# Kernel optimization log

Hardware: AMD Instinct MI355X
Metric: run time of the kernel (lower is better)

The kernel has to match this reference:

```python
import jax, jax.numpy as jnp
import numpy as np

B, S, D, H = 2, 2048, 1024, 16
DK = D // H
ROPE_BASE = 10000.0


def setup_inputs() -> dict:
    key = jax.random.key(0)
    ks = jax.random.split(key, 6)
    x = jax.random.normal(ks[0], (B, S, D), dtype=jnp.float32)
    # causal mask, broadcastable to [B,H,S,S]; masked_fill where mask==0
    mask = jnp.tril(jnp.ones((S, S), dtype=bool))[None, None]
    position_ids = jnp.tile(jnp.arange(S, dtype=jnp.int32)[None, :], (B, 1))
    sc = 1.0 / np.sqrt(D)
    Wq = jax.random.normal(ks[1], (D, D), dtype=jnp.float32) * sc
    Wk = jax.random.normal(ks[2], (D, D), dtype=jnp.float32) * sc
    Wv = jax.random.normal(ks[3], (D, D), dtype=jnp.float32) * sc
    Wo = jax.random.normal(ks[4], (D, D), dtype=jnp.float32) * sc
    bo = jnp.zeros((D,), dtype=jnp.float32)
    return {"x": x, "mask": mask, "position_ids": position_ids,
            "Wq": Wq, "Wk": Wk, "Wv": Wv, "Wo": Wo, "bo": bo}


def _rotate_half(t):
    t1, t2 = t[..., : t.shape[-1] // 2], t[..., t.shape[-1] // 2:]
    return jnp.concatenate((-t2, t1), axis=-1)


def reference(x, mask, position_ids, Wq, Wk, Wv, Wo, bo):
    b, s, d = x.shape
    h, dk = H, DK
    scale = 1.0 / np.sqrt(dk)

    def proj(W):  # torch Linear: x @ W.T -> [b,h,s,dk]
        return (x @ W.T).reshape(b, s, h, dk).transpose(0, 2, 1, 3)

    Q, K, V = proj(Wq), proj(Wk), proj(Wv)

    # rotary tables (computed in fp32, matching RotaryEmbedding)
    inv_freq = 1.0 / (ROPE_BASE ** (jnp.arange(0, dk, 2, dtype=jnp.float32) / dk))
    t = jnp.arange(s, dtype=jnp.float32)
    freqs = jnp.outer(t, inv_freq)            # [s, dk/2]
    emb = jnp.concatenate((freqs, freqs), -1) # [s, dk]
    cos = jnp.cos(emb)[position_ids][:, None]  # [b,1,s,dk]
    sin = jnp.sin(emb)[position_ids][:, None]
    Q = Q * cos + _rotate_half(Q) * sin
    K = K * cos + _rotate_half(K) * sin

    scores = jnp.einsum('bhqd,bhkd->bhqk', Q, K) * scale
    scores = jnp.where(mask, scores, jnp.float32(-1e9))
    attn = jax.nn.softmax(scores, axis=-1)  # dropout is identity in eval
    out = jnp.einsum('bhqk,bhkd->bhqd', attn, V)
    out = out.transpose(0, 2, 1, 3).reshape(b, s, d)
    return out @ Wo.T + bo
```

## Files before the change

### kernel.cpp

```cpp
#include <hip/hip_runtime.h>
#include <hip/hip_bf16.h>
#include <cstdint>

#define BB 2
#define SS 2048
#define DD 1024
#define HH 16
#define DK 64
#define MROWS (BB*SS)
#define NQKV  (3*DD)

typedef __bf16 bf16x8 __attribute__((ext_vector_type(8)));
typedef float  f32x4  __attribute__((ext_vector_type(4)));
typedef float  f32x16 __attribute__((ext_vector_type(16)));
typedef unsigned u32x2 __attribute__((ext_vector_type(2)));

static __device__ __forceinline__ unsigned short f2bf(float f) {
    __bf16 h = (__bf16)f;
    return __builtin_bit_cast(unsigned short, h);
}
static __device__ __forceinline__ float bf2f(unsigned short u) {
    return (float)__builtin_bit_cast(__bf16, u);
}

#define GLOAD16(gsrc, ldst) \
    __builtin_amdgcn_global_load_lds((const __attribute__((address_space(1))) void*)(gsrc), \
                                     (__attribute__((address_space(3))) void*)(ldst), 16, 0, 0)

static __device__ __forceinline__ void pl32_swap(unsigned &x, unsigned &y) {
#if __has_builtin(__builtin_amdgcn_permlane32_swap)
    u32x2 r = __builtin_amdgcn_permlane32_swap(x, y, false, false);
    x = r[0]; y = r[1];
#else
    asm volatile("v_permlane32_swap_b32 %0, %1" : "+v"(x), "+v"(y));
#endif
}
static __device__ __forceinline__ float swap_half(float v, bool hi) {
    unsigned x = __builtin_bit_cast(unsigned, v), y = x;
    pl32_swap(x, y);
    return __builtin_bit_cast(float, hi ? x : y);
}
template<int BASE> static __device__ __forceinline__ bf16x8 cvt_chunk(const f32x16 &p) {
    unsigned x0, y0, x1, y1;
    asm("v_cvt_pk_bf16_f32 %0, %1, %2" : "=v"(x0) : "v"(p[BASE+0]), "v"(p[BASE+1]));
    asm("v_cvt_pk_bf16_f32 %0, %1, %2" : "=v"(y0) : "v"(p[BASE+4]), "v"(p[BASE+5]));
    asm("v_cvt_pk_bf16_f32 %0, %1, %2" : "=v"(x1) : "v"(p[BASE+2]), "v"(p[BASE+3]));
    asm("v_cvt_pk_bf16_f32 %0, %1, %2" : "=v"(y1) : "v"(p[BASE+6]), "v"(p[BASE+7]));
    pl32_swap(x0, y0);
    pl32_swap(x1, y1);
    union { unsigned u[4]; bf16x8 v; } r;
    r.u[0] = x0; r.u[1] = x1; r.u[2] = y0; r.u[3] = y1;
    return r.v;
}

__global__ void cast_all(const float* __restrict__ x,  const float* __restrict__ wq,
                         const float* __restrict__ wk, const float* __restrict__ wv,
                         const float* __restrict__ wo,
                         unsigned short* __restrict__ xb, unsigned short* __restrict__ wqkv,
                         unsigned short* __restrict__ wob)
{
    const int NX = MROWS * DD;
    const int NW = DD * DD;
    const int total = (NX + 4 * NW) / 8;
    for (int i = blockIdx.x * blockDim.x + threadIdx.x; i < total; i += gridDim.x * blockDim.x) {
        int base = i * 8;
        const float* src; unsigned short* dst; int off;
        if      (base < NX)          { src = x;  dst = xb;          off = base; }
        else if (base < NX + NW)     { src = wq; dst = wqkv;        off = base - NX; }
        else if (base < NX + 2*NW)   { src = wk; dst = wqkv + NW;   off = base - NX - NW; }
        else if (base < NX + 3*NW)   { src = wv; dst = wqkv + 2*NW; off = base - NX - 2*NW; }
        else                         { src = wo; dst = wob;         off = base - NX - 3*NW; }
        float4 a = *(const float4*)(src + off);
        float4 b = *(const float4*)(src + off + 4);
        union { unsigned short s[8]; uint4 v; } u;
        u.s[0] = f2bf(a.x); u.s[1] = f2bf(a.y); u.s[2] = f2bf(a.z); u.s[3] = f2bf(a.w);
        u.s[4] = f2bf(b.x); u.s[5] = f2bf(b.y); u.s[6] = f2bf(b.z); u.s[7] = f2bf(b.w);
        *(uint4*)(dst + off) = u.v;
    }
}

__global__ void rope_table(float* __restrict__ tabc, float* __restrict__ tabs)
{
    int i = blockIdx.x * blockDim.x + threadIdx.x;
    int s = i >> 5, d = i & 31;
    float inv = exp2f(-(float)d * (13.287712379549449f / 32.f));
    float ang = (float)s * inv;
    tabc[i] = cosf(ang);
    tabs[i] = sinf(ang);
}

__global__ __launch_bounds__(512) void gemm_qkv(
    const unsigned short* __restrict__ A, const unsigned short* __restrict__ Bm,
    const int* __restrict__ pids,
    const float* __restrict__ tabc, const float* __restrict__ tabs,
    unsigned short* __restrict__ Qb, unsigned short* __restrict__ Kb,
    unsigned short* __restrict__ Vr)
{
    __shared__ __align__(16) unsigned short sA[2][16384];
    __shared__ __align__(16) unsigned short sB[2][16384];
    const int tid = threadIdx.x;
    const int w = tid >> 6, l = tid & 63;
    const int wm = w >> 2, wn = w & 3;
    const int lr = l & 15, lg = l >> 4;
    const int swz = (blockIdx.x & 7) * 24 + (blockIdx.x >> 3);
    const int bx = swz % 12, by = swz / 12;
    const int mBase = by * 256;
    const int sr  = tid >> 3;
    const int scb = (tid & 7) * 8;
    const int sksw = scb ^ ((sr & 7) * 8);
    const int rdsw = (lr & 7) * 8;

    f32x4 acc[8][4] = {};

    auto stage = [&](int kt, int bb) {
        #pragma unroll
        for (int r = 0; r < 4; ++r) {
            GLOAD16(A  + (size_t)(mBase + r*64 + sr) * DD + kt + sksw,
                    &sA[bb][r*4096 + sr*64 + scb]);
            GLOAD16(Bm + (size_t)(bx*256 + r*64 + sr) * DD + kt + sksw,
                    &sB[bb][r*4096 + sr*64 + scb]);
        }
    };

    stage(0, 0);
    __syncthreads();

    for (int t = 0; t < 16; ++t) {
        const int cur = t & 1;
        #pragma unroll
        for (int p = 0; p < 4; ++p) {
            const int rh = p & 1, ks = p >> 1;
            bf16x8 af[4], bfv[4];
            #pragma unroll
            for (int rf = 0; rf < 4; ++rf) {
                int ra = wm*128 + rh*64 + rf*16 + lr;
                af[rf] = *(const bf16x8*)&sA[cur][ra*64 + ((ks*32 + lg*8) ^ rdsw)];
            }
            #pragma unroll
            for (int cf = 0; cf < 4; ++cf) {
                int rb = wn*64 + cf*16 + lr;
                bfv[cf] = *(const bf16x8*)&sB[cur][rb*64 + ((ks*32 + lg*8) ^ rdsw)];
            }
            if (p == 0 && t < 15) stage((t+1)*64, cur ^ 1);
            __builtin_amdgcn_s_barrier();
            __builtin_amdgcn_s_setprio(1);
            #pragma unroll
            for (int rf = 0; rf < 4; ++rf)
                #pragma unroll
                for (int cf = 0; cf < 4; ++cf)
                    acc[rh*4+rf][cf] = __builtin_amdgcn_mfma_f32_16x16x32_bf16(
                        af[rf], bfv[cf], acc[rh*4+rf][cf], 0, 0, 0);
            __builtin_amdgcn_s_setprio(0);
            if (p < 3) __builtin_amdgcn_s_barrier();
        }
        __syncthreads();
    }

    if (bx < 8) {
        const bool isQ = bx < 4;
        unsigned short* dst = isQ ? Qb : Kb;
        const float qsc = isQ ? 0.1803368801111244f : 1.0f;
        const int colbase = (bx & 3)*256 + wn*64;
        #pragma unroll
        for (int rr = 0; rr < 8; ++rr) {
            #pragma unroll
            for (int j = 0; j < 4; ++j) {
                int row = mBase + wm*128 + rr*16 + lg*4 + j;
                int pos = pids[row];
                #pragma unroll
                for (int cf = 0; cf < 2; ++cf) {
                    int d = cf*16 + lr;
                    float cc = tabc[pos*32 + d];
                    float sn = tabs[pos*32 + d];
                    float a  = acc[rr][cf][j];
                    float bb2 = acc[rr][cf+2][j];
                    dst[(size_t)row * DD + colbase + d]      = f2bf((a*cc - bb2*sn) * qsc);
                    dst[(size_t)row * DD + colbase + d + 32] = f2bf((bb2*cc + a*sn) * qsc);
                }
            }
        }
    } else {
        const int colbase = (bx - 8)*256 + wn*64;
        #pragma unroll
        for (int rr = 0; rr < 8; ++rr) {
            #pragma unroll
            for (int j = 0; j < 4; ++j) {
                int row = mBase + wm*128 + rr*16 + lg*4 + j;
                #pragma unroll
                for (int cf = 0; cf < 4; ++cf)
                    Vr[(size_t)row * DD + colbase + cf*16 + lr] = f2bf(acc[rr][cf][j]);
            }
        }
    }
}

__global__ __launch_bounds__(256) void gemm_bt(
    const unsigned short* __restrict__ A, const unsigned short* __restrict__ Bm,
    float* __restrict__ Cout, const float* __restrict__ bias,
    int M, int N, int K)
{
    __shared__ __align__(16) unsigned short sA[2][128 * 64];
    __shared__ __align__(16) unsigned short sB[2][128 * 64];
    const int tid = threadIdx.x;
    const int w = tid >> 6, l = tid & 63;
    const int wm = w >> 1, wn = w & 1;
    const int lr = l & 15, lg = l >> 4;
    const int nwg = gridDim.x;
    const int cpx = nwg >> 3;
    const int swz = (blockIdx.x & 7) * cpx + (blockIdx.x >> 3);
    const int nbx = N >> 7;
    const int bx = swz % nbx, by = swz / nbx;
    const int mBase = by * 128, nBase = bx * 128;
    const int srow = tid >> 3;
    const int skof = (tid & 7) * 8;

    f32x4 acc[4][4] = {};

    #pragma unroll
    for (int i = 0; i < 4; ++i) {
        GLOAD16(A  + (size_t)(mBase + i*32 + srow) * K + skof, &sA[0][i*2048 + w*512]);
        GLOAD16(Bm + (size_t)(nBase + i*32 + srow) * K + skof, &sB[0][i*2048 + w*512]);
    }
    int cur = 0;

    for (int kt = 0; kt < K; kt += 64) {
        __syncthreads();
        if (kt + 64 < K) {
            #pragma unroll
            for (int i = 0; i < 4; ++i) {
                GLOAD16(A  + (size_t)(mBase + i*32 + srow) * K + kt + 64 + skof, &sA[cur^1][i*2048 + w*512]);
                GLOAD16(Bm + (size_t)(nBase + i*32 + srow) * K + kt + 64 + skof, &sB[cur^1][i*2048 + w*512]);
            }
        }
        #pragma unroll
        for (int kk = 0; kk < 2; ++kk) {
            bf16x8 af[4], bfv[4];
            #pragma unroll
            for (int mi = 0; mi < 4; ++mi)
                af[mi] = *(const bf16x8*)&sA[cur][(wm*64 + mi*16 + lr)*64 + kk*32 + lg*8];
            #pragma unroll
            for (int ni = 0; ni < 4; ++ni)
                bfv[ni] = *(const bf16x8*)&sB[cur][(wn*64 + ni*16 + lr)*64 + kk*32 + lg*8];
            #pragma unroll
            for (int mi = 0; mi < 4; ++mi)
                #pragma unroll
                for (int ni = 0; ni < 4; ++ni)
                    acc[mi][ni] = __builtin_amdgcn_mfma_f32_16x16x32_bf16(af[mi], bfv[ni], acc[mi][ni], 0, 0, 0);
        }
        cur ^= 1;
    }
    #pragma unroll
    for (int mi = 0; mi < 4; ++mi) {
        #pragma unroll
        for (int j = 0; j < 4; ++j) {
            int row = mBase + wm*64 + mi*16 + lg*4 + j;
            #pragma unroll
            for (int ni = 0; ni < 4; ++ni) {
                int col = nBase + wn*64 + ni*16 + lr;
                Cout[(size_t)row * N + col] = acc[mi][ni][j] + bias[col];
            }
        }
    }
}

__global__ __launch_bounds__(256) void v_transpose(
    const unsigned short* __restrict__ Vr, unsigned short* __restrict__ Vt)
{
    __shared__ __align__(16) unsigned short sT[64 * 64];
    const int bh = blockIdx.y;
    const int st = blockIdx.x;
    const int b = bh >> 4, h = bh & 15;
    const int tid = threadIdx.x;
    #pragma unroll
    for (int i = 0; i < 2; ++i) {
        int c = tid + i*256;
        int s = c >> 3, cb = c & 7;
        const unsigned short* src = Vr + (size_t)(b*SS + st*64 + s) * DD + h*64 + cb*8;
        uint4 v = *(const uint4*)src;
        *(uint4*)&sT[s*64 + ((cb ^ (s >> 3)) * 8)] = v;
    }
    __syncthreads();
    #pragma unroll
    for (int i = 0; i < 2; ++i) {
        int c = tid + i*256;
        int d = c >> 3, sb = c & 7;
        union { unsigned short u[8]; uint4 v; } o;
        #pragma unroll
        for (int e = 0; e < 8; ++e) {
            int s = sb*8 + e;
            o.u[e] = sT[s*64 + (((d >> 3) ^ (s >> 3)) * 8) + (d & 7)];
        }
        *(uint4*)(Vt + (size_t)(bh*64 + d) * SS + st*64 + sb*8) = o.v;
    }
}

__global__ __launch_bounds__(256, 4) void attn_fwd(
    const unsigned short* __restrict__ Qb,
    const unsigned short* __restrict__ Kb,
    const unsigned short* __restrict__ Vt,
    float* __restrict__ OpA,
    float* __restrict__ OpB,
    float* __restrict__ Ml)
{
    __shared__ __align__(16) unsigned short sK[2][4096];
    __shared__ __align__(16) unsigned short sV[2][4096];
    const int tid = threadIdx.x;
    const int w = tid >> 6, l = tid & 63;
    const int lq = l & 31;
    const int hi5 = l >> 5;
    const bool hb = hi5 != 0;

    const int xcd  = blockIdx.x & 7;
    const int c    = blockIdx.x >> 3;
    const int gsel = (c >> 1) & 3;
    const int half = c & 1;
    const int t2   = c >> 3;
    const int qt   = (t2 < 8) ? t2 : 23 - t2;
    const int bh   = xcd * 4 + gsel;
    const int b = bh >> 4, h = bh & 15;

    const int srow = tid >> 3;
    const int skof = (tid & 7) * 8;
    const int sksw = skof ^ ((srow & 7) * 8);
    const int sw   = (lq & 7) * 8;
    const float THR = 12.0f;

    bf16x8 qf[4];
    {
        const unsigned short* qp = Qb + (size_t)(b*SS + qt*128 + w*32 + lq) * DD + h*64 + hi5*8;
        #pragma unroll
        for (int dkc = 0; dkc < 4; ++dkc)
            qf[dkc] = *(const bf16x8*)(qp + dkc*16);
    }
    const int q_lane = qt*128 + w*32 + lq;
    const int wbase  = qt*128 + w*32;
    const int kt0    = half * (qt + 1);
    const int nsub   = qt + 1;

    f32x16 o0 = {}, o1 = {};
    float mrow = -3.0e38f, lsum = 0.f;
    int cur = 0;

    auto stage = [&](int kt, int bb) {
        #pragma unroll
        for (int r = 0; r < 2; ++r) {
            GLOAD16(Kb + (size_t)(b*SS + kt*64 + r*32 + srow) * DD + h*64 + sksw,
                    &sK[bb][r*2048 + w*512]);
            GLOAD16(Vt + (size_t)(bh*64 + r*32 + srow) * SS + kt*64 + sksw,
                    &sV[bb][r*2048 + w*512]);
        }
    };

    stage(kt0, 0);

    for (int s = 0; s < nsub; ++s) {
        const int kt = kt0 + s;
        __syncthreads();
        if (s + 1 < nsub) stage(kt + 1, cur ^ 1);

        f32x16 p0 = {}, p1 = {};
        __builtin_amdgcn_s_setprio(1);
        #pragma unroll
        for (int dkc = 0; dkc < 4; ++dkc) {
            bf16x8 k0 = *(const bf16x8*)&sK[cur][lq*64 + ((dkc*16 + hi5*8) ^ sw)];
            p0 = __builtin_amdgcn_mfma_f32_32x32x16_bf16(k0, qf[dkc], p0, 0, 0, 0);
        }
        #pragma unroll
        for (int dkc = 0; dkc < 4; ++dkc) {
            bf16x8 k1 = *(const bf16x8*)&sK[cur][2048 + lq*64 + ((dkc*16 + hi5*8) ^ sw)];
            p1 = __builtin_amdgcn_mfma_f32_32x32x16_bf16(k1, qf[dkc], p1, 0, 0, 0);
        }
        __builtin_amdgcn_s_setprio(0);

        if (kt*64 + 63 > wbase) {
            const int kb0 = kt*64 + 4*hi5;
            #pragma unroll
            for (int r = 0; r < 16; ++r) {
                const int cr = (r & 3) + 8*(r >> 2);
                if (kb0 + cr > q_lane)      p0[r] = -1e30f;
                if (kb0 + 32 + cr > q_lane) p1[r] = -1e30f;
            }
        }

        float tt[16];
        #pragma unroll
        for (int r = 0; r < 16; ++r) tt[r] = fmaxf(p0[r], p1[r]);
        #pragma unroll
        for (int s2 = 8; s2 >= 1; s2 >>= 1)
            #pragma unroll
            for (int r = 0; r < 8; ++r)
                if (r < s2) tt[r] = fmaxf(tt[r], tt[r + s2]);
        float tmx = fmaxf(tt[0], swap_half(tt[0], hb));

        float growth = tmx - mrow;
        if (!__all(growth <= THR)) {
            float mnew = fmaxf(mrow, tmx);
            float alpha = exp2f(mrow - mnew);
            lsum *= alpha;
            mrow = mnew;
            #pragma unroll
            for (int r = 0; r < 16; ++r) { o0[r] *= alpha; o1[r] *= alpha; }
        }

        #pragma unroll
        for (int r = 0; r < 16; ++r) {
            p0[r] = exp2f(p0[r] - mrow);
            p1[r] = exp2f(p1[r] - mrow);
        }
        float st[16];
        #pragma unroll
        for (int r = 0; r < 16; ++r) st[r] = p0[r] + p1[r];
        #pragma unroll
        for (int s2 = 8; s2 >= 1; s2 >>= 1)
            #pragma unroll
            for (int r = 0; r < 8; ++r)
                if (r < s2) st[r] += st[r + s2];
        lsum += st[0];

        __builtin_amdgcn_s_setprio(1);
        {
            bf16x8 pv, vf;
            pv = cvt_chunk<0>(p0);
            vf = *(const bf16x8*)&sV[cur][lq*64 + ((0*16 + hi5*8) ^ sw)];
            o0 = __builtin_amdgcn_mfma_f32_32x32x16_bf16(vf, pv, o0, 0, 0, 0);
            vf = *(const bf16x8*)&sV[cur][2048 + lq*64 + ((0*16 + hi5*8) ^ sw)];
            o1 = __builtin_amdgcn_mfma_f32_32x32x16_bf16(vf, pv, o1, 0, 0, 0);
            pv = cvt_chunk<8>(p0);
            vf = *(const bf16x8*)&sV[cur][lq*64 + ((1*16 + hi5*8) ^ sw)];
            o0 = __builtin_amdgcn_mfma_f32_32x32x16_bf16(vf, pv, o0, 0, 0, 0);
            vf = *(const bf16x8*)&sV[cur][2048 + lq*64 + ((1*16 + hi5*8) ^ sw)];
            o1 = __builtin_amdgcn_mfma_f32_32x32x16_bf16(vf, pv, o1, 0, 0, 0);
            pv = cvt_chunk<0>(p1);
            vf = *(const bf16x8*)&sV[cur][lq*64 + ((2*16 + hi5*8) ^ sw)];
            o0 = __builtin_amdgcn_mfma_f32_32x32x16_bf16(vf, pv, o0, 0, 0, 0);
            vf = *(const bf16x8*)&sV[cur][2048 + lq*64 + ((2*16 + hi5*8) ^ sw)];
            o1 = __builtin_amdgcn_mfma_f32_32x32x16_bf16(vf, pv, o1, 0, 0, 0);
            pv = cvt_chunk<8>(p1);
            vf = *(const bf16x8*)&sV[cur][lq*64 + ((3*16 + hi5*8) ^ sw)];
            o0 = __builtin_amdgcn_mfma_f32_32x32x16_bf16(vf, pv, o0, 0, 0, 0);
            vf = *(const bf16x8*)&sV[cur][2048 + lq*64 + ((3*16 + hi5*8) ^ sw)];
            o1 = __builtin_amdgcn_mfma_f32_32x32x16_bf16(vf, pv, o1, 0, 0, 0);
        }
        __builtin_amdgcn_s_setprio(0);
        cur ^= 1;
    }

    __syncthreads();
    float ls = lsum + swap_half(lsum, hb);
    float* sOf = (w < 2) ? (float*)&sK[w][0] : (float*)&sV[w - 2][0];

    #pragma unroll
    for (int g2 = 0; g2 < 4; ++g2) {
        f32x4 t0, t1;
        #pragma unroll
        for (int j = 0; j < 4; ++j) { t0[j] = o0[g2*4 + j]; t1[j] = o1[g2*4 + j]; }
        *(f32x4*)&sOf[lq*64 + g2*8 + hi5*4]      = t0;
        *(f32x4*)&sOf[lq*64 + 32 + g2*8 + hi5*4] = t1;
    }
    asm volatile("s_waitcnt lgkmcnt(0)" ::: "memory");
    __builtin_amdgcn_sched_barrier(0);

    float* Op = half ? OpB : OpA;
    const int row = l >> 1, cb2 = (l & 1) * 32;
    const float* sOr = sOf + row*64 + cb2;
    float* gp = Op + (size_t)(b*SS + qt*128 + w*32 + row) * DD + h*64 + cb2;
    #pragma unroll
    for (int c2 = 0; c2 < 8; ++c2)
        *(f32x4*)(gp + c2*4) = *(const f32x4*)(sOr + c2*4);

    if (!hb) {
        int qrow = qt*128 + w*32 + lq;
        float* mlp = Ml + (((size_t)half*32 + bh)*2048 + qrow)*2;
        mlp[0] = mrow;
        mlp[1] = ls;
    }
}

__global__ __launch_bounds__(256) void attn_merge(
    const float* __restrict__ OpA, const float* __restrict__ OpB,
    const float* __restrict__ Ml, unsigned short* __restrict__ Ob)
{
    int e = blockIdx.x * 256 + threadIdx.x;
    int row = e >> 8;
    int col = (e & 255) * 4;
    int b = row >> 11, q = row & 2047;
    int h = col >> 6;
    int bh = b*16 + h;
    const float* mlA = Ml + ((size_t)bh*2048 + q)*2;
    const float* mlB = Ml + (((size_t)32 + bh)*2048 + q)*2;
    float mA = mlA[0], lA = mlA[1];
    float mB = mlB[0], lB = mlB[1];
    float m  = fmaxf(mA, mB);
    float sA = exp2f(mA - m), sB = exp2f(mB - m);
    float linv = 1.f / (lA*sA + lB*sB);
    float fa = sA * linv, fb = sB * linv;
    f32x4 a = *(const f32x4*)(OpA + (size_t)e*4);
    f32x4 bq = *(const f32x4*)(OpB + (size_t)e*4);
    union { unsigned short s[4]; uint2 v; } o;
    #pragma unroll
    for (int j = 0; j < 4; ++j)
        o.s[j] = f2bf(a[j]*fa + bq[j]*fb);
    *(uint2*)(Ob + (size_t)e*4) = o.v;
}

extern "C" void kernel_launch(void* const* d_in, const int* in_sizes, int n_in,
                              void* d_out, int out_size, void* d_ws, size_t ws_size,
                              hipStream_t stream)
{
    const float* x  = (const float*)d_in[0];
    const int* pids = (const int*)d_in[2];
    const float* wq = (const float*)d_in[3];
    const float* wk = (const float*)d_in[4];
    const float* wv = (const float*)d_in[5];
    const float* wo = (const float*)d_in[6];
    const float* bo = (const float*)d_in[7];
    float* out = (float*)d_out;

    char* ws = (char*)d_ws;
    unsigned short* xb   = (unsigned short*)(ws);
    unsigned short* wqkv = (unsigned short*)(ws + (size_t)( 8u<<20));
    unsigned short* wob  = (unsigned short*)(ws + (size_t)(14u<<20));
    unsigned short* Vr   = (unsigned short*)(ws + (size_t)(16u<<20));
    float* Ml            = (float*)(ws + (size_t)(16u<<20));
    float* OpA           = (float*)(ws + (size_t)(24u<<20));
    unsigned short* Qb   = (unsigned short*)(ws + (size_t)(40u<<20));
    unsigned short* Kb   = (unsigned short*)(ws + (size_t)(48u<<20));
    unsigned short* Vt   = (unsigned short*)(ws + (size_t)(56u<<20));
    float* tabc          = (float*)(ws + (size_t)(64u<<20));
    float* tabs          = (float*)(ws + (size_t)(64u<<20) + (256u<<10));
    float* OpB           = out;
    unsigned short* Ob   = xb;

    cast_all<<<dim3(4096), dim3(256), 0, stream>>>(x, wq, wk, wv, wo, xb, wqkv, wob);
    rope_table<<<dim3(256), dim3(256), 0, stream>>>(tabc, tabs);
    gemm_qkv<<<dim3(192), dim3(512), 0, stream>>>(
        xb, wqkv, pids, tabc, tabs, Qb, Kb, Vr);
    v_transpose<<<dim3(32, 32), dim3(256), 0, stream>>>(Vr, Vt);
    attn_fwd<<<dim3(1024), dim3(256), 0, stream>>>(Qb, Kb, Vt, OpA, OpB, Ml);
    attn_merge<<<dim3(4096), dim3(256), 0, stream>>>(OpA, OpB, Ml, Ob);
    gemm_bt<<<dim3(256), dim3(256), 0, stream>>>(
        Ob, wob, out, bo, MROWS, DD, DD);
}
```

Before: 135.1 us.

## Use 4-slot K=32 ring buffer with 3-stage prefetch in QKV GEMM

Replaces the QKV projection GEMM's double-buffered K=64 stages with a four-slot ring of K=32 half-tiles. Each slot is prefetched three iterations ahead, and explicit vmcnt waits replace the per-phase syncthreads. The LDS swizzle changes to an XOR over 4 chunks per 32-wide row. The aim is to hide global load latency better and cut barriers per iteration. The cost is fewer MFMAs between barriers, and the swizzle may allow more LDS bank conflicts.

```diff
diff --git a/kernel.cpp b/kernel.cpp
--- a/kernel.cpp
+++ b/kernel.cpp
@@ -96,8 +96,8 @@
     unsigned short* __restrict__ Qb, unsigned short* __restrict__ Kb,
     unsigned short* __restrict__ Vr)
 {
-    __shared__ __align__(16) unsigned short sA[2][16384];
-    __shared__ __align__(16) unsigned short sB[2][16384];
+    __shared__ __align__(16) unsigned short sA[4][8192];
+    __shared__ __align__(16) unsigned short sB[4][8192];
     const int tid = threadIdx.x;
     const int w = tid >> 6, l = tid & 63;
     const int wm = w >> 2, wn = w & 3;
@@ -105,55 +105,51 @@
     const int swz = (blockIdx.x & 7) * 24 + (blockIdx.x >> 3);
     const int bx = swz % 12, by = swz / 12;
     const int mBase = by * 256;
-    const int sr  = tid >> 3;
-    const int scb = (tid & 7) * 8;
-    const int sksw = scb ^ ((sr & 7) * 8);
-    const int rdsw = (lr & 7) * 8;
+    const int nBase = bx * 256;
+    const int srow = tid >> 2;
+    const int schw = tid & 3;
 
     f32x4 acc[8][4] = {};
 
-    auto stage = [&](int kt, int bb) {
-        #pragma unroll
-        for (int r = 0; r < 4; ++r) {
-            GLOAD16(A  + (size_t)(mBase + r*64 + sr) * DD + kt + sksw,
-                    &sA[bb][r*4096 + sr*64 + scb]);
-            GLOAD16(Bm + (size_t)(bx*256 + r*64 + sr) * DD + kt + sksw,
-                    &sB[bb][r*4096 + sr*64 + scb]);
+    auto stage = [&](int kh) {
+        const int slot = kh & 3;
+        const int kbase = (kh >> 1) * 64 + (kh & 1) * 32;
+        #pragma unroll
+        for (int r = 0; r < 2; ++r) {
+            int row = r * 128 + srow;
+            int scol = kbase + ((schw ^ (row & 3)) * 8);
+            GLOAD16(A  + (size_t)(mBase + row) * DD + scol, &sA[slot][r*4096 + tid*8]);
+            GLOAD16(Bm + (size_t)(nBase + row) * DD + scol, &sB[slot][r*4096 + tid*8]);
         }
     };
 
-    stage(0, 0);
-    __syncthreads();
-
-    for (int t = 0; t < 16; ++t) {
-        const int cur = t & 1;
-        #pragma unroll
-        for (int p = 0; p < 4; ++p) {
-            const int rh = p & 1, ks = p >> 1;
-            bf16x8 af[4], bfv[4];
-            #pragma unroll
-            for (int rf = 0; rf < 4; ++rf) {
-                int ra = wm*128 + rh*64 + rf*16 + lr;
-                af[rf] = *(const bf16x8*)&sA[cur][ra*64 + ((ks*32 + lg*8) ^ rdsw)];
-            }
-            #pragma unroll
-            for (int cf = 0; cf < 4; ++cf) {
-                int rb = wn*64 + cf*16 + lr;
-                bfv[cf] = *(const bf16x8*)&sB[cur][rb*64 + ((ks*32 + lg*8) ^ rdsw)];
-            }
-            if (p == 0 && t < 15) stage((t+1)*64, cur ^ 1);
-            __builtin_amdgcn_s_barrier();
-            __builtin_amdgcn_s_setprio(1);
-            #pragma unroll
-            for (int rf = 0; rf < 4; ++rf)
-                #pragma unroll
-                for (int cf = 0; cf < 4; ++cf)
-                    acc[rh*4+rf][cf] = __builtin_amdgcn_mfma_f32_16x16x32_bf16(
-                        af[rf], bfv[cf], acc[rh*4+rf][cf], 0, 0, 0);
-            __builtin_amdgcn_s_setprio(0);
-            if (p < 3) __builtin_amdgcn_s_barrier();
-        }
-        __syncthreads();
+    stage(0); stage(1); stage(2);
+
+    for (int n = 0; n < 32; ++n) {
+        if (n == 31) { asm volatile("s_waitcnt vmcnt(0)" ::: "memory"); }
+        else         { asm volatile("s_waitcnt vmcnt(4)" ::: "memory"); }
+        __builtin_amdgcn_s_barrier();
+        if (n + 3 < 32) stage(n + 3);
+        const int slot = n & 3;
+        bf16x8 af[8], bfv[4];
+        #pragma unroll
+        for (int rf = 0; rf < 8; ++rf) {
+            int ra = wm*128 + rf*16 + lr;
+            af[rf] = *(const bf16x8*)&sA[slot][ra*32 + ((lg ^ (ra & 3)) * 8)];
+        }
+        #pragma unroll
+        for (int cf = 0; cf < 4; ++cf) {
+            int rb = wn*64 + cf*16 + lr;
+            bfv[cf] = *(const bf16x8*)&sB[slot][rb*32 + ((lg ^ (rb & 3)) * 8)];
+        }
+        __builtin_amdgcn_s_setprio(1);
+        #pragma unroll
+        for (int rf = 0; rf < 8; ++rf)
+            #pragma unroll
+            for (int cf = 0; cf < 4; ++cf)
+                acc[rf][cf] = __builtin_amdgcn_mfma_f32_16x16x32_bf16(
+                    af[rf], bfv[cf], acc[rf][cf], 0, 0, 0);
+        __builtin_amdgcn_s_setprio(0);
     }
 
     if (bx < 8) {
```

New measurement: 141.8 us. +5.0%, slower.
